# Kernel tuning notes

Measured on AMD Instinct MI355X. Metric: run time of the kernel, lower is better.

Reference implementation:

```python
import jax, jax.numpy as jnp
import numpy as np

B, S, H, E, D, K = 2, 4096, 1024, 8, 2048, 2


def setup_inputs() -> dict:
    key = jax.random.key(0)
    ks = jax.random.split(key, 6)
    scale = 0.02
    return {
        "x": jax.random.normal(ks[0], (B, S, H), dtype=jnp.float32),
        "gate_w": jax.random.normal(ks[1], (E, H), dtype=jnp.float32) * scale,
        "w1": jax.random.normal(ks[2], (E, H, D), dtype=jnp.float32) * scale,
        "b1": jnp.zeros((E, D), dtype=jnp.float32),
        "w2": jax.random.normal(ks[3], (E, D, H), dtype=jnp.float32) * scale,
        "b2": jnp.zeros((E, H), dtype=jnp.float32),
    }


def reference(x, gate_w, w1, b1, w2, b2):
    b, s, h = x.shape
    e = gate_w.shape[0]
    # Router
    router_logits = jnp.einsum('bsh,eh->bse', x, gate_w)
    router_probs = jax.nn.softmax(router_logits, axis=-1)
    top_k_probs, expert_idx = jax.lax.top_k(router_probs, K)      # [B,S,K]
    top_k_probs = top_k_probs / top_k_probs.sum(axis=-1, keepdims=True)
    # Aux load-balancing loss (faithful to source: mean over batch only -> [S,E])
    oh = jax.nn.one_hot(expert_idx, e, dtype=x.dtype)             # [B,S,K,E]
    tokens_per_expert = oh.sum(axis=-2).mean(axis=0)              # [S,E]
    avg_prob = router_probs.mean(axis=(0, 1))                     # [E]
    aux_loss = e * (tokens_per_expert * avg_prob).sum()
    # Dense combine weights per token per expert: [B*S, E]
    combine = (oh * top_k_probs[..., None]).sum(axis=-2).reshape(-1, e)
    # Expert MLPs, batched over experts (grouped GEMM form)
    xf = x.reshape(-1, h)                                         # [T,H]
    hid = jax.nn.gelu(jnp.einsum('th,ehd->etd', xf, w1) + b1[:, None, :],
                      approximate=False)                          # [E,T,D]
    y = jnp.einsum('etd,edh->eth', hid, w2) + b2[:, None, :]      # [E,T,H]
    out = jnp.einsum('te,eth->th', combine, y)                    # [T,H]
    return out.reshape(b, s, h), aux_loss
```

## Files before the change

kernel.cpp:

```cpp
#include <hip/hip_runtime.h>
#include <hip/hip_bf16.h>
#include <math.h>

#define Bdim 2
#define Sdim 4096
#define Hdim 1024
#define Edim 8
#define Ddim 2048
#define Tdim (Bdim*Sdim)

typedef __attribute__((ext_vector_type(8))) __bf16 bfv8;
typedef __attribute__((ext_vector_type(8))) short s16x8;
typedef __attribute__((ext_vector_type(4))) short s16x4;
typedef __attribute__((ext_vector_type(4))) float f32x4;

__device__ __forceinline__ short f2bf(float f) {
    union { float f; unsigned u; } a; a.f = f;
    unsigned r = (a.u + 0x7fffu + ((a.u >> 16) & 1u)) >> 16;
    return (short)r;
}
__device__ __forceinline__ float bf2f(short s) {
    union { unsigned u; float f; } a; a.u = ((unsigned)(unsigned short)s) << 16;
    return a.f;
}
__device__ __forceinline__ float fgelu(float x) {
    float u = fminf(x * (1.5957691f + 0.07135481f * x * x), 60.0f);
    float t = __expf(u);
    return x * t / (t + 1.0f);
}

typedef const __attribute__((address_space(1))) unsigned int ga_u32;
typedef __attribute__((address_space(3))) unsigned int la_u32;

__device__ __forceinline__ void gl_lds16(const void* g, void* l) {
    __builtin_amdgcn_global_load_lds((ga_u32*)g, (la_u32*)l, 16, 0, 0);
}

#define G_RD(SLOT) do {                                                              \
    _Pragma("unroll") for (int n = 0; n < 4; ++n)                                    \
        bf[n] = *(const bfv8*)(lds + 32768 + (SLOT) * 8192 + offB[n]);               \
    _Pragma("unroll") for (int m = 0; m < 8; ++m)                                    \
        af[m] = *(const bfv8*)(lds + (SLOT) * 8192 + offA[m]);                       \
    __builtin_amdgcn_sched_barrier(0);                                               \
} while (0)

#define G_MM() do {                                                                  \
    __builtin_amdgcn_s_setprio(1);                                                   \
    _Pragma("unroll") for (int m = 0; m < 8; ++m)                                    \
        _Pragma("unroll") for (int n = 0; n < 4; ++n)                                \
            acc[m][n] = __builtin_amdgcn_mfma_f32_16x16x32_bf16(af[m], bf[n], acc[m][n], 0, 0, 0); \
    __builtin_amdgcn_s_setprio(0);                                                   \
    __builtin_amdgcn_sched_barrier(0);                                               \
} while (0)

#define PH_S(SRD, SST) do {                                                          \
    G_RD(SRD);                                                                       \
    stage(SST);                                                                      \
    asm volatile("s_waitcnt vmcnt(8) lgkmcnt(0)" ::: "memory");                      \
    __builtin_amdgcn_s_barrier();                                                    \
    __builtin_amdgcn_sched_barrier(0);                                               \
    G_MM();                                                                          \
} while (0)

#define PH_T4(SRD) do {                                                              \
    G_RD(SRD);                                                                       \
    asm volatile("s_waitcnt vmcnt(4) lgkmcnt(0)" ::: "memory");                      \
    __builtin_amdgcn_s_barrier();                                                    \
    __builtin_amdgcn_sched_barrier(0);                                               \
    G_MM();                                                                          \
} while (0)

#define PH_T0(SRD) do {                                                              \
    G_RD(SRD);                                                                       \
    asm volatile("s_waitcnt vmcnt(0) lgkmcnt(0)" ::: "memory");                      \
    __builtin_amdgcn_s_barrier();                                                    \
    __builtin_amdgcn_sched_barrier(0);                                               \
    G_MM();                                                                          \
} while (0)

#define PH_TL(SRD) do {                                                              \
    G_RD(SRD);                                                                       \
    G_MM();                                                                          \
} while (0)

__global__ __launch_bounds__(256) void router_kernel(
    const float* __restrict__ x, const float* __restrict__ gw,
    int* __restrict__ cnt, float* __restrict__ psum,
    int* __restrict__ ltok, float* __restrict__ lw,
    short* __restrict__ xb)
{
    __shared__ float gws[Edim * Hdim];
    __shared__ int   lcnt[Edim], gbase[Edim];
    __shared__ int   s_e[32], s_pos[32], s_tok[32];
    __shared__ float s_w[32];
    __shared__ float s_ps[4][8];

    int tid = threadIdx.x;
    for (int i = tid; i < Edim * Hdim / 4; i += 256)
        ((float4*)gws)[i] = ((const float4*)gw)[i];
    if (tid < Edim) lcnt[tid] = 0;
    __syncthreads();

    int wave = tid >> 6, lane = tid & 63;
    float ps = 0.f;

    for (int i = 0; i < 4; ++i) {
        int t = blockIdx.x * 16 + wave * 4 + i;
        double acc[Edim];
#pragma unroll
        for (int e = 0; e < Edim; ++e) acc[e] = 0.0;
#pragma unroll
        for (int kq = 0; kq < 4; ++kq) {
            float4 xv = *(const float4*)(x + (size_t)t * Hdim + kq * 256 + lane * 4);
            if (xb) {
                s16x4 h; h[0]=f2bf(xv.x); h[1]=f2bf(xv.y); h[2]=f2bf(xv.z); h[3]=f2bf(xv.w);
                *(s16x4*)(xb + (size_t)t * Hdim + kq * 256 + lane * 4) = h;
            }
#pragma unroll
            for (int e = 0; e < Edim; ++e) {
                float4 wv = *(const float4*)(&gws[e * Hdim + kq * 256 + lane * 4]);
                acc[e] += (double)xv.x * wv.x + (double)xv.y * wv.y
                        + (double)xv.z * wv.z + (double)xv.w * wv.w;
            }
        }
#pragma unroll
        for (int e = 0; e < Edim; ++e) {
            acc[e] += __shfl_xor(acc[e], 1, 64);
            acc[e] += __shfl_xor(acc[e], 2, 64);
            acc[e] += __shfl_xor(acc[e], 4, 64);
        }
        int el = lane & 7;
        double v = acc[0];
#pragma unroll
        for (int e = 1; e < Edim; ++e) if (el == e) v = acc[e];
        v += __shfl_xor(v, 8, 64);
        v += __shfl_xor(v, 16, 64);
        v += __shfl_xor(v, 32, 64);
        double mx = v;
        mx = fmax(mx, __shfl_xor(mx, 1, 64));
        mx = fmax(mx, __shfl_xor(mx, 2, 64));
        mx = fmax(mx, __shfl_xor(mx, 4, 64));
        float ex = __expf((float)(v - mx));
        float sm = ex;
        sm += __shfl_xor(sm, 1, 64);
        sm += __shfl_xor(sm, 2, 64);
        sm += __shfl_xor(sm, 4, 64);
        ps += ex / sm;
        double le[8];
#pragma unroll
        for (int e = 0; e < 8; ++e) le[e] = __shfl(v, e, 8);
        if (lane == 0) {
            int e1 = 0;
#pragma unroll
            for (int e = 1; e < 8; ++e) if (le[e] > le[e1]) e1 = e;
            int e2 = -1;
#pragma unroll
            for (int e = 0; e < 8; ++e) {
                if (e == e1) continue;
                if (e2 < 0 || le[e] > le[e2]) e2 = e;
            }
            float r = __expf((float)(le[e2] - le[e1]));
            float w1v = 1.0f / (1.0f + r);
            int lt = (wave * 4 + i) * 2;
            int p1 = atomicAdd(&lcnt[e1], 1);
            s_e[lt] = e1; s_pos[lt] = p1; s_tok[lt] = 2*t;     s_w[lt] = w1v;
            int p2 = atomicAdd(&lcnt[e2], 1);
            s_e[lt+1] = e2; s_pos[lt+1] = p2; s_tok[lt+1] = 2*t+1; s_w[lt+1] = 1.0f - w1v;
        }
    }
    if (lane < 8) s_ps[wave][lane] = ps;
    __syncthreads();
    if (tid < 8) {
        atomicAdd(&psum[tid], s_ps[0][tid] + s_ps[1][tid] + s_ps[2][tid] + s_ps[3][tid]);
        gbase[tid] = atomicAdd(&cnt[tid], lcnt[tid]);
    }
    __syncthreads();
    if (tid < 32) {
        int e = s_e[tid];
        int pos = gbase[e] + s_pos[tid];
        ltok[e * Tdim + pos] = s_tok[tid];
        lw[e * Tdim + pos] = s_w[tid];
    }
}

__global__ void aux_kernel(const int* __restrict__ cnt,
                           const float* __restrict__ psum,
                           int* __restrict__ eoff,
                           float* __restrict__ out_aux)
{
    if (threadIdx.x == 0 && blockIdx.x == 0) {
        double s = 0.0;
        int run = 0;
        for (int e = 0; e < Edim; ++e) {
            eoff[e] = run;
            run += cnt[e];
            s += ((double)cnt[e] / (double)Bdim) * ((double)psum[e] / (double)Tdim);
        }
        out_aux[0] = (float)((double)Edim * s);
    }
}

__global__ __launch_bounds__(256) void convt2_kernel(
    const float* __restrict__ w1, const float* __restrict__ w2,
    short* __restrict__ w1t, short* __restrict__ w2t)
{
    int z = blockIdx.z;
    const float* w; short* wt; int R, C, r0, c0, e;
    if (z < 8) { e = z;     w = w1; wt = w1t; R = Hdim; C = Ddim; r0 = blockIdx.y * 64; c0 = blockIdx.x * 64; }
    else       { e = z - 8; w = w2; wt = w2t; R = Ddim; C = Hdim; r0 = blockIdx.x * 64; c0 = blockIdx.y * 64; }

    __shared__ short t[64][76];
    int tid = threadIdx.x;
    {
        int r = tid >> 2, cs = (tid & 3) * 16;
        const float* src = w + ((size_t)e * R + r0 + r) * C + c0 + cs;
#pragma unroll
        for (int q = 0; q < 4; ++q) {
            float4 v = *(const float4*)(src + q * 4);
            s16x4 h; h[0]=f2bf(v.x); h[1]=f2bf(v.y); h[2]=f2bf(v.z); h[3]=f2bf(v.w);
            *(s16x4*)(&t[r][cs + q * 4]) = h;
        }
    }
    __syncthreads();
    {
        int c = tid >> 2, rs = (tid & 3) * 16;
        short tmp[16];
#pragma unroll
        for (int j = 0; j < 16; ++j) tmp[j] = t[rs + j][c];
        short* dst = wt + ((size_t)e * C + c0 + c) * R + r0 + rs;
        *(s16x8*)dst = *(s16x8*)tmp;
        *(s16x8*)(dst + 8) = *(s16x8*)(tmp + 8);
    }
}


__global__ __launch_bounds__(512, 2) void gemm1n_kernel(
    const short* __restrict__ xb, const short* __restrict__ w1t,
    const float* __restrict__ b1, const int* __restrict__ cnt,
    const int* __restrict__ eoff, const int* __restrict__ ltok,
    short* __restrict__ hid)
{
    constexpr int GXN = Ddim / 256;
    int id = blockIdx.x;
    int e = id & 7;
    unsigned rem = (unsigned)id >> 3;
    int bx = rem & (GXN - 1);
    int by = rem / GXN;

    int n_e = cnt[e];
    int row0 = by * 256;
    if (row0 >= n_e) return;
    int col0 = bx * 256;
    int slot0 = eoff[e];

    __shared__ short lds[65536];
    char* ldsb = (char*)lds;

    int tid = threadIdx.x;
    int w = tid >> 6, lane = tid & 63;

    const short* aS[2]; const short* bS[2];
    int oD[2];
#pragma unroll
    for (int j = 0; j < 2; ++j) {
        int o = tid * 16 + j * 8192;
        oD[j] = o;
        int eff = o ^ (((o >> 7) & 7) << 4);
        int row = ((eff >> 7) << 1) | ((eff >> 6) & 1);
        int kB  = eff & 63;
        int gr = row0 + row; if (gr > n_e - 1) gr = n_e - 1;
        int tok = ltok[(size_t)e * Tdim + gr] >> 1;
        aS[j] = xb + (size_t)tok * Hdim + (kB >> 1);
        bS[j] = w1t + ((size_t)e * Ddim + col0 + row) * Hdim + (kB >> 1);
    }

    int fr = lane & 15, kg = lane >> 4;
    int wm = (w >> 2) * 128, wn = (w & 3) * 64;

    int offA[8], offB[4];
#pragma unroll
    for (int m = 0; m < 8; ++m) {
        int r = wm + m * 16 + fr;
        offA[m] = (r >> 1) * 64 + ((((r & 1) * 32) + kg * 8) ^ (((r >> 1) & 7) << 3));
    }
#pragma unroll
    for (int n = 0; n < 4; ++n) {
        int r = wn + n * 16 + fr;
        offB[n] = (r >> 1) * 64 + ((((r & 1) * 32) + kg * 8) ^ (((r >> 1) & 7) << 3));
    }

    f32x4 acc[8][4];
#pragma unroll
    for (int m = 0; m < 8; ++m)
#pragma unroll
        for (int n = 0; n < 4; ++n) acc[m][n] = (f32x4)0.0f;

    bfv8 af[8], bf[4];

    auto stage = [&](int s) {
#pragma unroll
        for (int j = 0; j < 2; ++j) {
            gl_lds16(aS[j], ldsb + s * 16384 + oD[j]);
            aS[j] += 32;
            gl_lds16(bS[j], ldsb + 65536 + s * 16384 + oD[j]);
            bS[j] += 32;
        }
    };

    constexpr int NH = Hdim / 32;
    stage(0); stage(1); stage(2);
    asm volatile("s_waitcnt vmcnt(8)" ::: "memory");
    __builtin_amdgcn_s_barrier();
    __builtin_amdgcn_sched_barrier(0);
#pragma unroll 1
    for (int it = 0; it < (NH - 4) / 4; ++it) {
        PH_S(0, 3); PH_S(1, 0); PH_S(2, 1); PH_S(3, 2);
    }
    PH_S(0, 3);
    PH_T4(1);
    PH_T0(2);
    PH_TL(3);

#pragma unroll
    for (int m = 0; m < 8; ++m) {
        int r0r = wm + m * 16 + kg * 4;
#pragma unroll
        for (int j = 0; j < 4; ++j) {
            int gr = row0 + r0r + j;
            if (gr >= n_e) continue;
            size_t hbase = (size_t)(slot0 + gr) * Ddim;
#pragma unroll
            for (int n = 0; n < 4; ++n) {
                int col = col0 + wn + n * 16 + fr;
                float v = acc[m][n][j] + b1[e * Ddim + col];
                hid[hbase + col] = f2bf(fgelu(v));
            }
        }
    }
}

__global__ __launch_bounds__(512, 2) void gemm2n_kernel(
    const short* __restrict__ hid, const short* __restrict__ w2t,
    const float* __restrict__ b2, const int* __restrict__ cnt,
    const int* __restrict__ eoff, const int* __restrict__ ltok,
    const float* __restrict__ lw, short* __restrict__ out2)
{
    constexpr int GXN = Hdim / 256;
    int id = blockIdx.x;
    int e = id & 7;
    unsigned rem = (unsigned)id >> 3;
    int bx = rem & (GXN - 1);
    int by = rem / GXN;

    int n_e = cnt[e];
    int row0 = by * 256;
    if (row0 >= n_e) return;
    int col0 = bx * 256;
    int slot0 = eoff[e];

    __shared__ short lds[65536];
    char* ldsb = (char*)lds;

    int tid = threadIdx.x;
    int w = tid >> 6, lane = tid & 63;

    const short* aS[2]; const short* bS[2];
    int oD[2];
#pragma unroll
    for (int j = 0; j < 2; ++j) {
        int o = tid * 16 + j * 8192;
        oD[j] = o;
        int eff = o ^ (((o >> 7) & 7) << 4);
        int row = ((eff >> 7) << 1) | ((eff >> 6) & 1);
        int kB  = eff & 63;
        int gr = row0 + row; if (gr > n_e - 1) gr = n_e - 1;
        aS[j] = hid + (size_t)(slot0 + gr) * Ddim + (kB >> 1);
        bS[j] = w2t + ((size_t)e * Hdim + col0 + row) * Ddim + (kB >> 1);
    }

    int fr = lane & 15, kg = lane >> 4;
    int wm = (w >> 2) * 128, wn = (w & 3) * 64;

    int offA[8], offB[4];
#pragma unroll
    for (int m = 0; m < 8; ++m) {
        int r = wm + m * 16 + fr;
        offA[m] = (r >> 1) * 64 + ((((r & 1) * 32) + kg * 8) ^ (((r >> 1) & 7) << 3));
    }
#pragma unroll
    for (int n = 0; n < 4; ++n) {
        int r = wn + n * 16 + fr;
        offB[n] = (r >> 1) * 64 + ((((r & 1) * 32) + kg * 8) ^ (((r >> 1) & 7) << 3));
    }

    f32x4 acc[8][4];
#pragma unroll
    for (int m = 0; m < 8; ++m)
#pragma unroll
        for (int n = 0; n < 4; ++n) acc[m][n] = (f32x4)0.0f;

    bfv8 af[8], bf[4];

    auto stage = [&](int s) {
#pragma unroll
        for (int j = 0; j < 2; ++j) {
            gl_lds16(aS[j], ldsb + s * 16384 + oD[j]);
            aS[j] += 32;
            gl_lds16(bS[j], ldsb + 65536 + s * 16384 + oD[j]);
            bS[j] += 32;
        }
    };

    constexpr int NH = Ddim / 32;
    stage(0); stage(1); stage(2);
    asm volatile("s_waitcnt vmcnt(8)" ::: "memory");
    __builtin_amdgcn_s_barrier();
    __builtin_amdgcn_sched_barrier(0);
#pragma unroll 1
    for (int it = 0; it < (NH - 4) / 4; ++it) {
        PH_S(0, 3); PH_S(1, 0); PH_S(2, 1); PH_S(3, 2);
    }
    PH_S(0, 3);
    PH_T4(1);
    PH_T0(2);
    PH_TL(3);

#pragma unroll
    for (int m = 0; m < 8; ++m) {
        int r0r = wm + m * 16 + kg * 4;
#pragma unroll
        for (int j = 0; j < 4; ++j) {
            int gr = row0 + r0r + j;
            if (gr >= n_e) continue;
            int val = ltok[(size_t)e * Tdim + gr];
            float p = lw[(size_t)e * Tdim + gr];
            size_t obase = (size_t)val * Hdim;
#pragma unroll
            for (int n = 0; n < 4; ++n) {
                int col = col0 + wn + n * 16 + fr;
                float v = p * (acc[m][n][j] + b2[e * Hdim + col]);
                out2[obase + col] = f2bf(v);
            }
        }
    }
}

__global__ __launch_bounds__(256) void combine_kernel(const short* __restrict__ out2,
                                                      float* __restrict__ out)
{
    size_t i = ((size_t)blockIdx.x * 256 + threadIdx.x) * 8;
    size_t t = i >> 10;
    int h = (int)(i & 1023);
    s16x8 a = *(const s16x8*)(out2 + (t * 2) * 1024 + h);
    s16x8 b = *(const s16x8*)(out2 + (t * 2 + 1) * 1024 + h);
    float4 o0, o1;
    o0.x = bf2f(a[0]) + bf2f(b[0]); o0.y = bf2f(a[1]) + bf2f(b[1]);
    o0.z = bf2f(a[2]) + bf2f(b[2]); o0.w = bf2f(a[3]) + bf2f(b[3]);
    o1.x = bf2f(a[4]) + bf2f(b[4]); o1.y = bf2f(a[5]) + bf2f(b[5]);
    o1.z = bf2f(a[6]) + bf2f(b[6]); o1.w = bf2f(a[7]) + bf2f(b[7]);
    *(float4*)(out + i) = o0;
    *(float4*)(out + i + 4) = o1;
}

#define FBK 64
#define FLDK 72

__global__ __launch_bounds__(256) void gemm1_fb(
    const float* __restrict__ x, const float* __restrict__ w1,
    const float* __restrict__ b1, const int* __restrict__ cnt,
    const int* __restrict__ ltok, short* __restrict__ hid,
    int CH, int row_base)
{
    int e = blockIdx.z;
    int n_e = cnt[e];
    int row0 = row_base + blockIdx.y * 128;
    if (row0 >= n_e) return;
    int col0 = blockIdx.x * 128;

    __shared__ short As[128][FLDK];
    __shared__ short Bs[128][FLDK];

    int tid = threadIdx.x;
    int arow = tid >> 1;
    int akh  = (tid & 1) * 32;
    int gr_a = row0 + arow;
    int tok = ltok[(size_t)e * Tdim + (gr_a < n_e ? gr_a : n_e - 1)] >> 1;
    const float* xrow = x + (size_t)tok * Hdim + akh;
    int bdg = (tid & 31) * 4;
    int bkg = (tid >> 5) * 4;

    int lane = tid & 63;
    int wid = tid >> 6;
    int wm = (wid >> 1) * 64, wn = (wid & 1) * 64;
    int fr = lane & 15, kg = lane >> 4;

    f32x4 acc[4][4];
#pragma unroll
    for (int m = 0; m < 4; ++m)
#pragma unroll
        for (int n = 0; n < 4; ++n) acc[m][n] = (f32x4)0.0f;

    const float* wB = w1 + (size_t)e * Hdim * Ddim + col0;

    for (int k0 = 0; k0 < Hdim; k0 += FBK) {
#pragma unroll
        for (int i = 0; i < 8; ++i) {
            float4 v = *(const float4*)(xrow + k0 + i * 4);
            s16x4 h; h[0] = f2bf(v.x); h[1] = f2bf(v.y); h[2] = f2bf(v.z); h[3] = f2bf(v.w);
            *(s16x4*)(&As[arow][akh + i * 4]) = h;
        }
#pragma unroll
        for (int r = 0; r < 2; ++r) {
            int kq = bkg + r * 32;
            float4 v0 = *(const float4*)(wB + (size_t)(k0 + kq + 0) * Ddim + bdg);
            float4 v1 = *(const float4*)(wB + (size_t)(k0 + kq + 1) * Ddim + bdg);
            float4 v2 = *(const float4*)(wB + (size_t)(k0 + kq + 2) * Ddim + bdg);
            float4 v3 = *(const float4*)(wB + (size_t)(k0 + kq + 3) * Ddim + bdg);
            const float* p0 = (const float*)&v0; const float* p1 = (const float*)&v1;
            const float* p2 = (const float*)&v2; const float* p3 = (const float*)&v3;
#pragma unroll
            for (int c = 0; c < 4; ++c) {
                s16x4 h; h[0] = f2bf(p0[c]); h[1] = f2bf(p1[c]); h[2] = f2bf(p2[c]); h[3] = f2bf(p3[c]);
                *(s16x4*)(&Bs[bdg + c][kq]) = h;
            }
        }
        __syncthreads();
        bfv8 af[4][2], bfr[4][2];
#pragma unroll
        for (int m = 0; m < 4; ++m)
#pragma unroll
            for (int kk = 0; kk < 2; ++kk)
                af[m][kk] = *(const bfv8*)(&As[wm + m * 16 + fr][kk * 32 + kg * 8]);
#pragma unroll
        for (int n = 0; n < 4; ++n)
#pragma unroll
            for (int kk = 0; kk < 2; ++kk)
                bfr[n][kk] = *(const bfv8*)(&Bs[wn + n * 16 + fr][kk * 32 + kg * 8]);
#pragma unroll
        for (int m = 0; m < 4; ++m)
#pragma unroll
            for (int n = 0; n < 4; ++n) {
                acc[m][n] = __builtin_amdgcn_mfma_f32_16x16x32_bf16(af[m][0], bfr[n][0], acc[m][n], 0, 0, 0);
                acc[m][n] = __builtin_amdgcn_mfma_f32_16x16x32_bf16(af[m][1], bfr[n][1], acc[m][n], 0, 0, 0);
            }
        __syncthreads();
    }

    int lr0 = row0 - row_base;
#pragma unroll
    for (int m = 0; m < 4; ++m) {
        int r0r = wm + m * 16 + kg * 4;
#pragma unroll
        for (int j = 0; j < 4; ++j) {
            int gr = row0 + r0r + j;
            if (gr >= n_e) continue;
            size_t hbase = ((size_t)e * CH + (size_t)(lr0 + r0r + j)) * Ddim;
#pragma unroll
            for (int n = 0; n < 4; ++n) {
                int col = col0 + wn + n * 16 + fr;
                float v = acc[m][n][j] + b1[e * Ddim + col];
                float g = 0.5f * v * (1.0f + erff(v * 0.70710678118654752440f));
                hid[hbase + col] = f2bf(g);
            }
        }
    }
}

__global__ __launch_bounds__(256) void gemm2_fb(
    const short* __restrict__ hid, const float* __restrict__ w2,
    const float* __restrict__ b2, const int* __restrict__ cnt,
    const int* __restrict__ ltok, const float* __restrict__ lw,
    float* __restrict__ out, int CH, int row_base)
{
    int e = blockIdx.z;
    int n_e = cnt[e];
    int row0 = row_base + blockIdx.y * 128;
    if (row0 >= n_e) return;
    int col0 = blockIdx.x * 128;

    __shared__ short As[128][FLDK];
    __shared__ short Bs[128][FLDK];

    int tid = threadIdx.x;
    int arow = tid >> 1;
    int akh  = (tid & 1) * 32;
    const short* hrow = hid + ((size_t)e * CH + (size_t)(row0 - row_base + arow)) * Ddim + akh;
    int bdg = (tid & 31) * 4;
    int bkg = (tid >> 5) * 4;

    int lane = tid & 63;
    int wid = tid >> 6;
    int wm = (wid >> 1) * 64, wn = (wid & 1) * 64;
    int fr = lane & 15, kg = lane >> 4;

    f32x4 acc[4][4];
#pragma unroll
    for (int m = 0; m < 4; ++m)
#pragma unroll
        for (int n = 0; n < 4; ++n) acc[m][n] = (f32x4)0.0f;

    const float* wB = w2 + (size_t)e * Ddim * Hdim + col0;

    for (int k0 = 0; k0 < Ddim; k0 += FBK) {
#pragma unroll
        for (int i = 0; i < 4; ++i) {
            s16x8 v = *(const s16x8*)(hrow + k0 + i * 8);
            *(s16x8*)(&As[arow][akh + i * 8]) = v;
        }
#pragma unroll
        for (int r = 0; r < 2; ++r) {
            int kq = bkg + r * 32;
            float4 v0 = *(const float4*)(wB + (size_t)(k0 + kq + 0) * Hdim + bdg);
            float4 v1 = *(const float4*)(wB + (size_t)(k0 + kq + 1) * Hdim + bdg);
            float4 v2 = *(const float4*)(wB + (size_t)(k0 + kq + 2) * Hdim + bdg);
            float4 v3 = *(const float4*)(wB + (size_t)(k0 + kq + 3) * Hdim + bdg);
            const float* p0 = (const float*)&v0; const float* p1 = (const float*)&v1;
            const float* p2 = (const float*)&v2; const float* p3 = (const float*)&v3;
#pragma unroll
            for (int c = 0; c < 4; ++c) {
                s16x4 h; h[0] = f2bf(p0[c]); h[1] = f2bf(p1[c]); h[2] = f2bf(p2[c]); h[3] = f2bf(p3[c]);
                *(s16x4*)(&Bs[bdg + c][kq]) = h;
            }
        }
        __syncthreads();
        bfv8 af[4][2], bfr[4][2];
#pragma unroll
        for (int m = 0; m < 4; ++m)
#pragma unroll
            for (int kk = 0; kk < 2; ++kk)
                af[m][kk] = *(const bfv8*)(&As[wm + m * 16 + fr][kk * 32 + kg * 8]);
#pragma unroll
        for (int n = 0; n < 4; ++n)
#pragma unroll
            for (int kk = 0; kk < 2; ++kk)
                bfr[n][kk] = *(const bfv8*)(&Bs[wn + n * 16 + fr][kk * 32 + kg * 8]);
#pragma unroll
        for (int m = 0; m < 4; ++m)
#pragma unroll
            for (int n = 0; n < 4; ++n) {
                acc[m][n] = __builtin_amdgcn_mfma_f32_16x16x32_bf16(af[m][0], bfr[n][0], acc[m][n], 0, 0, 0);
                acc[m][n] = __builtin_amdgcn_mfma_f32_16x16x32_bf16(af[m][1], bfr[n][1], acc[m][n], 0, 0, 0);
            }
        __syncthreads();
    }

#pragma unroll
    for (int m = 0; m < 4; ++m) {
        int r0r = wm + m * 16 + kg * 4;
#pragma unroll
        for (int j = 0; j < 4; ++j) {
            int gr = row0 + r0r + j;
            if (gr >= n_e) continue;
            int tok = ltok[(size_t)e * Tdim + gr] >> 1;
            float p = lw[(size_t)e * Tdim + gr];
#pragma unroll
            for (int n = 0; n < 4; ++n) {
                int col = col0 + wn + n * 16 + fr;
                float v = p * (acc[m][n][j] + b2[e * Hdim + col]);
                atomicAdd(&out[(size_t)tok * Hdim + col], v);
            }
        }
    }
}

extern "C" void kernel_launch(void* const* d_in, const int* in_sizes, int n_in,
                              void* d_out, int out_size, void* d_ws, size_t ws_size,
                              hipStream_t stream)
{
    const float* x  = (const float*)d_in[0];
    const float* gw = (const float*)d_in[1];
    const float* w1 = (const float*)d_in[2];
    const float* b1 = (const float*)d_in[3];
    const float* w2 = (const float*)d_in[4];
    const float* b2 = (const float*)d_in[5];
    float* out = (float*)d_out;

    char* wsb = (char*)d_ws;
    int*   cnt  = (int*)wsb;
    float* psum = (float*)(wsb + 32);
    int*   eoff = (int*)(wsb + 64);
    int*   ltok = (int*)(wsb + 128);
    float* lwp  = (float*)(wsb + 128 + (size_t)Edim * Tdim * 4);
    size_t lists_end = 128 + (size_t)Edim * Tdim * 8;

    size_t xb_sz = (size_t)Tdim * Hdim * 2;
    size_t w1t_sz = (size_t)Edim * Hdim * Ddim * 2;
    size_t w2t_sz = w1t_sz;
    size_t hid_sz = (size_t)(2 * Tdim) * Ddim * 2;
    size_t req = lists_end + xb_sz + w1t_sz + w2t_sz + hid_sz;

    hipMemsetAsync(wsb, 0, 128, stream);

    if (req <= ws_size) {
        short* xb   = (short*)(wsb + lists_end);
        short* w1t  = (short*)(wsb + lists_end + xb_sz);
        short* w2t  = (short*)(wsb + lists_end + xb_sz + w1t_sz);
        short* hid  = (short*)(wsb + lists_end + xb_sz + w1t_sz + w2t_sz);
        short* out2 = w1t;

        convt2_kernel<<<dim3(32, 16, 16), 256, 0, stream>>>(w1, w2, w1t, w2t);
        router_kernel<<<Tdim / 16, 256, 0, stream>>>(x, gw, cnt, psum, ltok, lwp, xb);
        aux_kernel<<<1, 64, 0, stream>>>(cnt, psum, eoff, out + (size_t)Tdim * Hdim);

        gemm1n_kernel<<<(Ddim / 256) * 32 * Edim, 512, 0, stream>>>(
            xb, w1t, b1, cnt, eoff, ltok, hid);
        gemm2n_kernel<<<(Hdim / 256) * 32 * Edim, 512, 0, stream>>>(
            hid, w2t, b2, cnt, eoff, ltok, lwp, out2);
        combine_kernel<<<(size_t)Tdim * Hdim / 2048, 256, 0, stream>>>(out2, out);
    } else {
        short* hid = (short*)(wsb + lists_end);
        int CH2 = 2048;
        while (CH2 > 128 && lists_end + (size_t)Edim * CH2 * Ddim * 2 > ws_size) CH2 >>= 1;

        hipMemsetAsync(d_out, 0, (size_t)out_size * 4, stream);
        router_kernel<<<Tdim / 16, 256, 0, stream>>>(x, gw, cnt, psum, ltok, lwp, nullptr);
        aux_kernel<<<1, 64, 0, stream>>>(cnt, psum, eoff, out + (size_t)Tdim * Hdim);

        int chunks = Tdim / CH2;
        for (int c = 0; c < chunks; ++c) {
            gemm1_fb<<<dim3(Ddim / 128, CH2 / 128, Edim), 256, 0, stream>>>(
                x, w1, b1, cnt, ltok, hid, CH2, c * CH2);
            gemm2_fb<<<dim3(Hdim / 128, CH2 / 128, Edim), 256, 0, stream>>>(
                hid, w2, b2, cnt, ltok, lwp, out, CH2, c * CH2);
        }
    }
}
```

Measured before the change: 328.5 us.

## Switch GEMMs to double-buffered LDS pipeline and shrink GEMM2 tile to 256x128

Both expert GEMM kernels drop the 4-stage LDS ring with partial vmcnt waits and use a 2-stage double buffer that issues the next stage's loads, computes the current one, then does a full vmcnt(0) wait and barrier. LDS per block is halved and launch bounds are raised to 4 blocks per CU to get more occupancy. GEMM2 also halves its output column tile to 128 with 4x4 accumulators per wave, doubling its grid. The cost is less prefetch depth, a full drain every K-step, and lower arithmetic intensity in GEMM2. A 4-block register budget may also cause spills with the 8x4 accumulator in GEMM1.

```diff
diff --git a/kernel.cpp b/kernel.cpp
--- a/kernel.cpp
+++ b/kernel.cpp
@@ -36,15 +36,20 @@
     __builtin_amdgcn_global_load_lds((ga_u32*)g, (la_u32*)l, 16, 0, 0);
 }
 
-#define G_RD(SLOT) do {                                                              \
+#define SYNC0() do {                                                     \
+    asm volatile("s_waitcnt vmcnt(0)" ::: "memory");                     \
+    __builtin_amdgcn_s_barrier();                                        \
+    __builtin_amdgcn_sched_barrier(0);                                   \
+} while (0)
+
+#define RD1(S) do {                                                                  \
     _Pragma("unroll") for (int n = 0; n < 4; ++n)                                    \
-        bf[n] = *(const bfv8*)(lds + 32768 + (SLOT) * 8192 + offB[n]);               \
+        bf[n] = *(const bfv8*)(lds + 16384 + (S) * 8192 + offB[n]);                  \
     _Pragma("unroll") for (int m = 0; m < 8; ++m)                                    \
-        af[m] = *(const bfv8*)(lds + (SLOT) * 8192 + offA[m]);                       \
+        af[m] = *(const bfv8*)(lds + (S) * 8192 + offA[m]);                          \
     __builtin_amdgcn_sched_barrier(0);                                               \
 } while (0)
-
-#define G_MM() do {                                                                  \
+#define MM1() do {                                                                   \
     __builtin_amdgcn_s_setprio(1);                                                   \
     _Pragma("unroll") for (int m = 0; m < 8; ++m)                                    \
         _Pragma("unroll") for (int n = 0; n < 4; ++n)                                \
@@ -52,36 +57,26 @@
     __builtin_amdgcn_s_setprio(0);                                                   \
     __builtin_amdgcn_sched_barrier(0);                                               \
 } while (0)
-
-#define PH_S(SRD, SST) do {                                                          \
-    G_RD(SRD);                                                                       \
-    stage(SST);                                                                      \
-    asm volatile("s_waitcnt vmcnt(8) lgkmcnt(0)" ::: "memory");                      \
-    __builtin_amdgcn_s_barrier();                                                    \
+#define PH1F(SST, SRD) do { stage(SST); RD1(SRD); MM1(); SYNC0(); } while (0)
+#define PH1L(SRD)      do { RD1(SRD); MM1(); } while (0)
+
+#define RD2(S) do {                                                                  \
+    _Pragma("unroll") for (int n = 0; n < 4; ++n)                                    \
+        bf[n] = *(const bfv8*)(lds + 16384 + (S) * 4096 + offB[n]);                  \
+    _Pragma("unroll") for (int m = 0; m < 4; ++m)                                    \
+        af[m] = *(const bfv8*)(lds + (S) * 8192 + offA[m]);                          \
     __builtin_amdgcn_sched_barrier(0);                                               \
-    G_MM();                                                                          \
 } while (0)
-
-#define PH_T4(SRD) do {                                                              \
-    G_RD(SRD);                                                                       \
-    asm volatile("s_waitcnt vmcnt(4) lgkmcnt(0)" ::: "memory");                      \
-    __builtin_amdgcn_s_barrier();                                                    \
+#define MM2() do {                                                                   \
+    __builtin_amdgcn_s_setprio(1);                                                   \
+    _Pragma("unroll") for (int m = 0; m < 4; ++m)                                    \
+        _Pragma("unroll") for (int n = 0; n < 4; ++n)                                \
+            acc[m][n] = __builtin_amdgcn_mfma_f32_16x16x32_bf16(af[m], bf[n], acc[m][n], 0, 0, 0); \
+    __builtin_amdgcn_s_setprio(0);                                                   \
     __builtin_amdgcn_sched_barrier(0);                                               \
-    G_MM();                                                                          \
 } while (0)
-
-#define PH_T0(SRD) do {                                                              \
-    G_RD(SRD);                                                                       \
-    asm volatile("s_waitcnt vmcnt(0) lgkmcnt(0)" ::: "memory");                      \
-    __builtin_amdgcn_s_barrier();                                                    \
-    __builtin_amdgcn_sched_barrier(0);                                               \
-    G_MM();                                                                          \
-} while (0)
-
-#define PH_TL(SRD) do {                                                              \
-    G_RD(SRD);                                                                       \
-    G_MM();                                                                          \
-} while (0)
+#define PH2F(SST, SRD) do { stage(SST); RD2(SRD); MM2(); SYNC0(); } while (0)
+#define PH2L(SRD)      do { RD2(SRD); MM2(); } while (0)
 
 __global__ __launch_bounds__(256) void router_kernel(
     const float* __restrict__ x, const float* __restrict__ gw,
@@ -233,8 +228,7 @@
     }
 }
 
-
-__global__ __launch_bounds__(512, 2) void gemm1n_kernel(
+__global__ __launch_bounds__(512, 4) void gemm1n_kernel(
     const short* __restrict__ xb, const short* __restrict__ w1t,
     const float* __restrict__ b1, const int* __restrict__ cnt,
     const int* __restrict__ eoff, const int* __restrict__ ltok,
@@ -253,7 +247,7 @@
     int col0 = bx * 256;
     int slot0 = eoff[e];
 
-    __shared__ short lds[65536];
+    __shared__ short lds[32768];
     char* ldsb = (char*)lds;
 
     int tid = threadIdx.x;
@@ -302,24 +296,21 @@
         for (int j = 0; j < 2; ++j) {
             gl_lds16(aS[j], ldsb + s * 16384 + oD[j]);
             aS[j] += 32;
-            gl_lds16(bS[j], ldsb + 65536 + s * 16384 + oD[j]);
+            gl_lds16(bS[j], ldsb + 32768 + s * 16384 + oD[j]);
             bS[j] += 32;
         }
     };
 
     constexpr int NH = Hdim / 32;
-    stage(0); stage(1); stage(2);
-    asm volatile("s_waitcnt vmcnt(8)" ::: "memory");
-    __builtin_amdgcn_s_barrier();
-    __builtin_amdgcn_sched_barrier(0);
+    stage(0);
+    SYNC0();
 #pragma unroll 1
-    for (int it = 0; it < (NH - 4) / 4; ++it) {
-        PH_S(0, 3); PH_S(1, 0); PH_S(2, 1); PH_S(3, 2);
-    }
-    PH_S(0, 3);
-    PH_T4(1);
-    PH_T0(2);
-    PH_TL(3);
+    for (int it = 0; it < (NH - 2) / 2; ++it) {
+        PH1F(1, 0);
+        PH1F(0, 1);
+    }
+    PH1F(1, 0);
+    PH1L(1);
 
 #pragma unroll
     for (int m = 0; m < 8; ++m) {
@@ -339,13 +330,13 @@
     }
 }
 
-__global__ __launch_bounds__(512, 2) void gemm2n_kernel(
+__global__ __launch_bounds__(512, 4) void gemm2n_kernel(
     const short* __restrict__ hid, const short* __restrict__ w2t,
     const float* __restrict__ b2, const int* __restrict__ cnt,
     const int* __restrict__ eoff, const int* __restrict__ ltok,
     const float* __restrict__ lw, short* __restrict__ out2)
 {
-    constexpr int GXN = Hdim / 256;
+    constexpr int GXN = Hdim / 128;
     int id = blockIdx.x;
     int e = id & 7;
     unsigned rem = (unsigned)id >> 3;
@@ -355,17 +346,17 @@
     int n_e = cnt[e];
     int row0 = by * 256;
     if (row0 >= n_e) return;
-    int col0 = bx * 256;
+    int col0 = bx * 128;
     int slot0 = eoff[e];
 
-    __shared__ short lds[65536];
+    __shared__ short lds[24576];
     char* ldsb = (char*)lds;
 
     int tid = threadIdx.x;
     int w = tid >> 6, lane = tid & 63;
 
-    const short* aS[2]; const short* bS[2];
-    int oD[2];
+    const short* aS[2]; const short* bS0;
+    int oD[2], oB;
 #pragma unroll
     for (int j = 0; j < 2; ++j) {
         int o = tid * 16 + j * 8192;
@@ -375,15 +366,22 @@
         int kB  = eff & 63;
         int gr = row0 + row; if (gr > n_e - 1) gr = n_e - 1;
         aS[j] = hid + (size_t)(slot0 + gr) * Ddim + (kB >> 1);
-        bS[j] = w2t + ((size_t)e * Hdim + col0 + row) * Ddim + (kB >> 1);
+    }
+    {
+        int o = tid * 16;
+        oB = o;
+        int eff = o ^ (((o >> 7) & 7) << 4);
+        int row = ((eff >> 7) << 1) | ((eff >> 6) & 1);
+        int kB  = eff & 63;
+        bS0 = w2t + ((size_t)e * Hdim + col0 + row) * Ddim + (kB >> 1);
     }
 
     int fr = lane & 15, kg = lane >> 4;
-    int wm = (w >> 2) * 128, wn = (w & 3) * 64;
-
-    int offA[8], offB[4];
-#pragma unroll
-    for (int m = 0; m < 8; ++m) {
+    int wm = (w >> 1) * 64, wn = (w & 1) * 64;
+
+    int offA[4], offB[4];
+#pragma unroll
+    for (int m = 0; m < 4; ++m) {
         int r = wm + m * 16 + fr;
         offA[m] = (r >> 1) * 64 + ((((r & 1) * 32) + kg * 8) ^ (((r >> 1) & 7) << 3));
     }
@@ -393,40 +391,37 @@
         offB[n] = (r >> 1) * 64 + ((((r & 1) * 32) + kg * 8) ^ (((r >> 1) & 7) << 3));
     }
 
-    f32x4 acc[8][4];
-#pragma unroll
-    for (int m = 0; m < 8; ++m)
+    f32x4 acc[4][4];
+#pragma unroll
+    for (int m = 0; m < 4; ++m)
 #pragma unroll
         for (int n = 0; n < 4; ++n) acc[m][n] = (f32x4)0.0f;
 
-    bfv8 af[8], bf[4];
+    bfv8 af[4], bf[4];
 
     auto stage = [&](int s) {
 #pragma unroll
         for (int j = 0; j < 2; ++j) {
             gl_lds16(aS[j], ldsb + s * 16384 + oD[j]);
             aS[j] += 32;
-            gl_lds16(bS[j], ldsb + 65536 + s * 16384 + oD[j]);
-            bS[j] += 32;
-        }
+        }
+        gl_lds16(bS0, ldsb + 32768 + s * 8192 + oB);
+        bS0 += 32;
     };
 
     constexpr int NH = Ddim / 32;
-    stage(0); stage(1); stage(2);
-    asm volatile("s_waitcnt vmcnt(8)" ::: "memory");
-    __builtin_amdgcn_s_barrier();
-    __builtin_amdgcn_sched_barrier(0);
+    stage(0);
+    SYNC0();
 #pragma unroll 1
-    for (int it = 0; it < (NH - 4) / 4; ++it) {
-        PH_S(0, 3); PH_S(1, 0); PH_S(2, 1); PH_S(3, 2);
-    }
-    PH_S(0, 3);
-    PH_T4(1);
-    PH_T0(2);
-    PH_TL(3);
-
-#pragma unroll
-    for (int m = 0; m < 8; ++m) {
+    for (int it = 0; it < (NH - 2) / 2; ++it) {
+        PH2F(1, 0);
+        PH2F(0, 1);
+    }
+    PH2F(1, 0);
+    PH2L(1);
+
+#pragma unroll
+    for (int m = 0; m < 4; ++m) {
         int r0r = wm + m * 16 + kg * 4;
 #pragma unroll
         for (int j = 0; j < 4; ++j) {
@@ -704,7 +699,7 @@
 
         gemm1n_kernel<<<(Ddim / 256) * 32 * Edim, 512, 0, stream>>>(
             xb, w1t, b1, cnt, eoff, ltok, hid);
-        gemm2n_kernel<<<(Hdim / 256) * 32 * Edim, 512, 0, stream>>>(
+        gemm2n_kernel<<<(Hdim / 128) * 32 * Edim, 512, 0, stream>>>(
             hid, w2t, b2, cnt, eoff, ltok, lwp, out2);
         combine_kernel<<<(size_t)Tdim * Hdim / 2048, 256, 0, stream>>>(out2, out);
     } else {
```

After: 1.215 ms. 270% more time.
